# Kernel optimization log

Measured on AMD Instinct MI355X. Metric: run time of the kernel, lower is better.

## Reference

```python
import jax, jax.numpy as jnp
import numpy as np

B, L, DM = 2, 2048, 2048
DI = 2 * DM          # d_inner = expand * d_model
N = 16               # d_state
K = 4                # d_conv
R = DM // 16         # dt_rank = ceil(d_model/16) = 128
FF = 8192            # intermediate_size
EPS = 1e-5


def _silu(x):
    return x * jax.nn.sigmoid(x)


def _ln(x, w, b):
    mu = jnp.mean(x, -1, keepdims=True)
    var = jnp.mean((x - mu) ** 2, -1, keepdims=True)
    return (x - mu) * jax.lax.rsqrt(var + EPS) * w + b


def setup_inputs() -> dict:
    key = jax.random.key(0)
    ks = jax.random.split(key, 8)

    def w(k, shape, fan_in):
        return jax.random.normal(k, shape, jnp.float32) / np.sqrt(fan_in).astype(np.float32)

    return {
        "hidden_states": jax.random.normal(ks[0], (B, L, DM), jnp.float32),
        "ln1_w": jnp.ones((DM,), jnp.float32),
        "ln1_b": jnp.zeros((DM,), jnp.float32),
        "W_in": w(ks[1], (2 * DI, DM), DM),      # in_proj (x and gate merged)
        "conv_w": w(ks[2], (DI, K), K),           # depthwise causal conv weights
        "conv_b": jnp.zeros((DI,), jnp.float32),
        "W_x": w(ks[3], (R + 2 * N, DI), DI),     # x_proj -> [dt_rank | B | C]
        "W_dt": w(ks[4], (DI, R), R),             # dt_proj (bias applied in scan)
        "b_dt": jnp.full((DI,), -2.0, jnp.float32),
        "A": -jnp.tile(jnp.arange(1.0, N + 1.0, dtype=jnp.float32), (DI, 1)),  # (DI, N)
        "Dp": jnp.ones((DI,), jnp.float32),
        "W_out": w(ks[5], (DM, DI), DI),
        "ln2_w": jnp.ones((DM,), jnp.float32),
        "ln2_b": jnp.zeros((DM,), jnp.float32),
        "W_fc1": w(ks[6], (2 * FF, DM), DM),      # GLU: [gate | y]
        "W_fc2": w(ks[7], (DM, FF), FF),
    }


def reference(hidden_states, ln1_w, ln1_b, W_in, conv_w, conv_b, W_x, W_dt, b_dt,
              A, Dp, W_out, ln2_w, ln2_b, W_fc1, W_fc2):
    # --- input layernorm + Phi4Mamba (prefill path: causal_conv1d_fn + selective_scan_fn) ---
    res = hidden_states
    x = _ln(hidden_states, ln1_w, ln1_b)

    xz = jnp.einsum('bld,ed->ble', x, W_in)           # (B, L, 2*DI)
    xs, gate = jnp.split(xz, 2, axis=-1)              # each (B, L, DI)

    # depthwise causal conv1d (width K) fused with silu
    xp = jnp.pad(xs, ((0, 0), (K - 1, 0), (0, 0)))
    conv = conv_b
    for k in range(K):
        conv = conv + xp[:, k:k + L, :] * conv_w[:, k]
    xs = _silu(conv)                                  # (B, L, DI)

    ssm = jnp.einsum('bld,ed->ble', xs, W_x)          # (B, L, R+2N)
    dt, Bm, Cm = ssm[..., :R], ssm[..., R:R + N], ssm[..., R + N:]
    delta = jax.nn.softplus(jnp.einsum('blr,dr->bld', dt, W_dt) + b_dt)  # (B, L, DI)

    def step(h, inp):
        d_t, b_t, c_t, x_t = inp                       # (B,DI),(B,N),(B,N),(B,DI)
        h = jnp.exp(d_t[..., None] * A) * h + (d_t * x_t)[..., None] * b_t[:, None, :]
        return h, jnp.einsum('bdn,bn->bd', h, c_t)

    h0 = jnp.zeros((B, DI, N), xs.dtype)
    _, ys = jax.lax.scan(step, h0, (delta.transpose(1, 0, 2), Bm.transpose(1, 0, 2),
                                    Cm.transpose(1, 0, 2), xs.transpose(1, 0, 2)))
    y = ys.transpose(1, 0, 2) + Dp * xs               # (B, L, DI)
    y = y * _silu(gate)                                # selective_scan z-gating
    attn_out = jnp.einsum('bld,ed->ble', y, W_out)    # (B, L, DM)

    hs = res + attn_out

    # --- post layernorm + GLU MLP ---
    res2 = hs
    x2 = _ln(hs, ln2_w, ln2_b)
    gy = jnp.einsum('bld,ed->ble', x2, W_fc1)         # (B, L, 2*FF)
    g, yy = jnp.split(gy, 2, axis=-1)
    mlp = jnp.einsum('blf,df->bld', yy * _silu(g), W_fc2)
    return res2 + mlp
```

## Files before the change

kernel.cpp:

```cpp
#include <hip/hip_runtime.h>
#include <hip/hip_bf16.h>

typedef unsigned short u16;
typedef unsigned int u32;

#define L_SEQ 2048
#define DMODEL 2048
#define DINNER 4096
#define NSTATE 16
#define MROWS 4096
#define CHUNK 32
#define NCHK  64

typedef __bf16 bf16x8 __attribute__((ext_vector_type(8)));
typedef float f32x4 __attribute__((ext_vector_type(4)));

__device__ __forceinline__ u16 f2bf(float f) {
    union { float f; u32 u; } v; v.f = f;
    u32 u = v.u;
    u32 r = (u + 0x7fffu + ((u >> 16) & 1u)) >> 16;
    return (u16)r;
}
__device__ __forceinline__ float bf2f(u16 h) {
    union { u32 u; float f; } v; v.u = ((u32)h) << 16;
    return v.f;
}

__device__ __forceinline__ void gload16(const void* g, void* l) {
    __builtin_amdgcn_global_load_lds((const __attribute__((address_space(1))) void*)g,
                                     (__attribute__((address_space(3))) void*)l, 16, 0, 0);
}

__global__ __launch_bounds__(256) void cvt_kernel(const float* __restrict__ src,
                                                  u16* __restrict__ dst, long nsrc) {
    long i = ((long)blockIdx.x * 256 + threadIdx.x) * 8;
    union { uint4 v; u16 u[8]; } o;
    if (i < nsrc) {
        f32x4 a = *(const f32x4*)(src + i);
        f32x4 b = *(const f32x4*)(src + i + 4);
#pragma unroll
        for (int j = 0; j < 4; ++j) { o.u[j] = f2bf(a[j]); o.u[4 + j] = f2bf(b[j]); }
    } else {
#pragma unroll
        for (int j = 0; j < 8; ++j) o.u[j] = 0;
    }
    *(uint4*)(dst + i) = o.v;
}

__global__ __launch_bounds__(256) void ln_kernel(const float* __restrict__ in,
                                                 const float* __restrict__ w,
                                                 const float* __restrict__ b,
                                                 u16* __restrict__ out) {
    const long row = blockIdx.x;
    const float* x = in + row * DMODEL;
    const int t = threadIdx.x;
    f32x4 v0 = *(const f32x4*)(x + t * 8);
    f32x4 v1 = *(const f32x4*)(x + t * 8 + 4);
    float s = 0.f, sq = 0.f;
#pragma unroll
    for (int j = 0; j < 4; ++j) {
        s += v0[j] + v1[j];
        sq += v0[j] * v0[j] + v1[j] * v1[j];
    }
#pragma unroll
    for (int off = 32; off > 0; off >>= 1) {
        s += __shfl_down(s, off);
        sq += __shfl_down(sq, off);
    }
    __shared__ float red[8];
    __shared__ float stats[2];
    const int wid = t >> 6, lane = t & 63;
    if (lane == 0) { red[wid] = s; red[4 + wid] = sq; }
    __syncthreads();
    if (t == 0) {
        float S = red[0] + red[1] + red[2] + red[3];
        float Q = red[4] + red[5] + red[6] + red[7];
        float mu = S / (float)DMODEL;
        stats[0] = mu;
        stats[1] = rsqrtf(Q / (float)DMODEL - mu * mu + 1e-5f);
    }
    __syncthreads();
    float mu = stats[0], rstd = stats[1];
    union { uint4 v; u16 u[8]; } o;
#pragma unroll
    for (int j = 0; j < 8; ++j) {
        float xv = (j < 4) ? v0[j] : v1[j - 4];
        o.u[j] = f2bf((xv - mu) * rstd * w[t * 8 + j] + b[t * 8 + j]);
    }
    *(uint4*)(out + row * DMODEL + t * 8) = o.v;
}

template <int MODE>
__global__ __launch_bounds__(256) void gemm_bt(const u16* __restrict__ A,
                                               const u16* __restrict__ W,
                                               float* __restrict__ Cf,
                                               u16* __restrict__ Cb,
                                               const float* __restrict__ addv,
                                               int M, int N, int K, int lda, int ldb) {
    __shared__ u16 As[128 * 64];
    __shared__ u16 Bs[128 * 64];
    const int tid = threadIdx.x;
    const int wid = tid >> 6;
    const int lane = tid & 63;
    const int m0 = blockIdx.y << 7;
    const int n0 = blockIdx.x << 7;
    const long koff = (long)blockIdx.z * K;
    const long zoff = (long)blockIdx.z * M * N;
    const int wr = (wid >> 1) << 6;
    const int wc = (wid & 1) << 6;
    const int l15 = lane & 15;
    const int lhi = lane >> 4;

    f32x4 acc[4][4];
#pragma unroll
    for (int i = 0; i < 4; ++i)
#pragma unroll
        for (int j = 0; j < 4; ++j) acc[i][j] = (f32x4){0.f, 0.f, 0.f, 0.f};

    const int srow = (wid << 3) + (lane >> 3);
    const int scol = (lane & 7) << 3;

    const u16* aBase = A + (long)(m0 + srow) * lda + scol + koff;
    const u16* bBase = W + (long)(n0 + srow) * (long)ldb + scol + koff;

    for (int k0 = 0; k0 < K; k0 += 64) {
#pragma unroll
        for (int i = 0; i < 4; ++i) {
            gload16(aBase + (long)(i * 32) * lda + k0, &As[((i << 5) + (wid << 3)) << 6]);
            gload16(bBase + (long)(i * 32) * ldb + k0, &Bs[((i << 5) + (wid << 3)) << 6]);
        }
        __syncthreads();
#pragma unroll
        for (int kk = 0; kk < 64; kk += 32) {
            bf16x8 af[4], bfr[4];
#pragma unroll
            for (int i = 0; i < 4; ++i)
                af[i] = *(const bf16x8*)&As[((wr + (i << 4) + l15) << 6) + kk + (lhi << 3)];
#pragma unroll
            for (int j = 0; j < 4; ++j)
                bfr[j] = *(const bf16x8*)&Bs[((wc + (j << 4) + l15) << 6) + kk + (lhi << 3)];
#pragma unroll
            for (int i = 0; i < 4; ++i)
#pragma unroll
                for (int j = 0; j < 4; ++j)
                    acc[i][j] = __builtin_amdgcn_mfma_f32_16x16x32_bf16(af[i], bfr[j], acc[i][j], 0, 0, 0);
        }
        __syncthreads();
    }

#pragma unroll
    for (int i = 0; i < 4; ++i) {
#pragma unroll
        for (int j = 0; j < 4; ++j) {
#pragma unroll
            for (int r = 0; r < 4; ++r) {
                int row = m0 + wr + (i << 4) + (lhi << 2) + r;
                int col = n0 + wc + (j << 4) + l15;
                long idx = (long)row * N + col;
                float v = acc[i][j][r];
                if (MODE == 2) v += addv[idx];
                if (MODE == 1) Cb[idx] = f2bf(v);
                else Cf[zoff + idx] = v;
            }
        }
    }
}

template <int MODE>
__global__ __launch_bounds__(512, 2) void gemm8(const u16* __restrict__ A,
                                                const u16* __restrict__ W,
                                                float* __restrict__ Cf,
                                                u16* __restrict__ Cb,
                                                const float* __restrict__ addv,
                                                int M, int N, int K, int lda, int ldb) {
    __shared__ u16 lds[4][2][256 * 32];
    const int tid = threadIdx.x;
    const int wid = tid >> 6;
    const int lane = tid & 63;
    const int wr = wid >> 2;
    const int wc = wid & 3;
    const int l15 = lane & 15;
    const int lhi = lane >> 4;
    const int sw = (l15 >> 1) & 3;
    const long koff = (long)blockIdx.z * K;
    const long zoff = (long)blockIdx.z * M * N;

    const int nwg = gridDim.x * gridDim.y;
    const int flat = blockIdx.y * gridDim.x + blockIdx.x;
    const int q8 = nwg >> 3, r8 = nwg & 7;
    const int xcd = flat & 7, lid = flat >> 3;
    const int swz = (xcd < r8 ? xcd * (q8 + 1) : r8 * (q8 + 1) + (xcd - r8) * q8) + lid;
    const int m0 = (swz / gridDim.x) << 8;
    const int n0 = (swz % gridDim.x) << 8;

    const int srow = lane >> 2;
    const int gc16 = (lane & 3) ^ ((lane >> 3) & 3);

    f32x4 acc[8][4];
#pragma unroll
    for (int i = 0; i < 8; ++i)
#pragma unroll
        for (int j = 0; j < 4; ++j) acc[i][j] = (f32x4){0.f, 0.f, 0.f, 0.f};

#define STAGE_A(t, j)                                                                              \
    gload16(A + (long)(m0 + (j) * 128 + wid * 16 + srow) * lda + koff + (long)(t) * 32 + gc16 * 8, \
            &lds[(t) & 3][0][((j) * 128 + wid * 16) * 32])
#define STAGE_B(t, j)                                                                              \
    gload16(W + (long)(n0 + (j) * 128 + wid * 16 + srow) * (long)ldb + koff + (long)(t) * 32 + gc16 * 8, \
            &lds[(t) & 3][1][((j) * 128 + wid * 16) * 32])

    STAGE_A(0, 0); STAGE_A(0, 1); STAGE_B(0, 0); STAGE_B(0, 1);
    STAGE_A(1, 0); STAGE_A(1, 1); STAGE_B(1, 0); STAGE_B(1, 1);
    STAGE_A(2, 0); STAGE_A(2, 1); STAGE_B(2, 0); STAGE_B(2, 1);
    asm volatile("s_waitcnt vmcnt(8)" ::: "memory");
    __builtin_amdgcn_s_barrier();
    __builtin_amdgcn_sched_barrier(0);

    const int nt = K >> 5;
    for (int t = 0; t < nt; ++t) {
        const u16* Ab = &lds[t & 3][0][0];
        const u16* Bb = &lds[t & 3][1][0];
        bf16x8 afrg[4], bfrg[4];
#pragma unroll
        for (int f = 0; f < 4; ++f)
            afrg[f] = *(const bf16x8*)&Ab[(wr * 128 + f * 16 + l15) * 32 + ((lhi ^ sw) << 3)];
#pragma unroll
        for (int f = 0; f < 4; ++f)
            bfrg[f] = *(const bf16x8*)&Bb[(wc * 64 + f * 16 + l15) * 32 + ((lhi ^ sw) << 3)];
        if (t + 3 < nt) { STAGE_A(t + 3, 0); STAGE_A(t + 3, 1); }
        __builtin_amdgcn_s_barrier();
        __builtin_amdgcn_s_setprio(1);
#pragma unroll
        for (int i = 0; i < 4; ++i)
#pragma unroll
            for (int j = 0; j < 4; ++j)
                acc[i][j] = __builtin_amdgcn_mfma_f32_16x16x32_bf16(afrg[i], bfrg[j], acc[i][j], 0, 0, 0);
        __builtin_amdgcn_s_setprio(0);
#pragma unroll
        for (int f = 0; f < 4; ++f)
            afrg[f] = *(const bf16x8*)&Ab[(wr * 128 + (f + 4) * 16 + l15) * 32 + ((lhi ^ sw) << 3)];
        if (t + 3 < nt) { STAGE_B(t + 3, 0); STAGE_B(t + 3, 1); }
        __builtin_amdgcn_s_barrier();
        __builtin_amdgcn_s_setprio(1);
#pragma unroll
        for (int i = 0; i < 4; ++i)
#pragma unroll
            for (int j = 0; j < 4; ++j)
                acc[i + 4][j] = __builtin_amdgcn_mfma_f32_16x16x32_bf16(afrg[i], bfrg[j], acc[i + 4][j], 0, 0, 0);
        __builtin_amdgcn_s_setprio(0);
        const int rem = nt - 2 - t;
        if (rem >= 2)      { asm volatile("s_waitcnt vmcnt(8)" ::: "memory"); }
        else if (rem == 1) { asm volatile("s_waitcnt vmcnt(4)" ::: "memory"); }
        else if (rem == 0) { asm volatile("s_waitcnt vmcnt(0)" ::: "memory"); }
        __builtin_amdgcn_s_barrier();
        __builtin_amdgcn_sched_barrier(0);
    }
#undef STAGE_A
#undef STAGE_B

#pragma unroll
    for (int i = 0; i < 8; ++i) {
#pragma unroll
        for (int j = 0; j < 4; ++j) {
#pragma unroll
            for (int r = 0; r < 4; ++r) {
                int row = m0 + wr * 128 + i * 16 + lhi * 4 + r;
                int col = n0 + wc * 64 + j * 16 + l15;
                long idx = (long)row * N + col;
                float v = acc[i][j][r];
                if (MODE == 2) v += addv[idx];
                if (MODE == 1) Cb[idx] = f2bf(v);
                else Cf[zoff + idx] = v;
            }
        }
    }
}

__global__ __launch_bounds__(256) void reduce_add_kernel(const float* __restrict__ p0,
                                                         const float* __restrict__ p1,
                                                         const float* __restrict__ add,
                                                         float* __restrict__ out) {
    long i = ((long)blockIdx.x * 256 + threadIdx.x) * 4;
    f32x4 a = *(const f32x4*)(p0 + i);
    f32x4 b = *(const f32x4*)(p1 + i);
    f32x4 c = *(const f32x4*)(add + i);
    f32x4 o;
#pragma unroll
    for (int j = 0; j < 4; ++j) o[j] = a[j] + b[j] + c[j];
    *(f32x4*)(out + i) = o;
}

__global__ __launch_bounds__(256) void reduce4_bf16_kernel(const float* __restrict__ p,
                                                           u16* __restrict__ outb) {
    long i = ((long)blockIdx.x * 256 + threadIdx.x) * 4;
    const long S = 4096L * 256;
    f32x4 a = *(const f32x4*)(p + i);
    f32x4 b = *(const f32x4*)(p + S + i);
    f32x4 c = *(const f32x4*)(p + 2 * S + i);
    f32x4 d = *(const f32x4*)(p + 3 * S + i);
    union { uint2 v; u16 u[4]; } o;
#pragma unroll
    for (int j = 0; j < 4; ++j) o.u[j] = f2bf(a[j] + b[j] + c[j] + d[j]);
    *(uint2*)(outb + i) = o.v;
}

__global__ __launch_bounds__(256) void conv_silu_kernel(const u16* __restrict__ xz,
                                                        const float* __restrict__ cw,
                                                        const float* __restrict__ cb,
                                                        float* __restrict__ xs_out,
                                                        u16* __restrict__ act_out) {
    const int d0 = (blockIdx.x * 256 + threadIdx.x) * 8;
    const int bl = blockIdx.y;
    const int l = bl & (L_SEQ - 1);
    float acc[8];
    float wt[8][4];
#pragma unroll
    for (int j = 0; j < 8; ++j) {
        f32x4 wj = *(const f32x4*)(cw + (d0 + j) * 4);
        wt[j][0] = wj[0]; wt[j][1] = wj[1]; wt[j][2] = wj[2]; wt[j][3] = wj[3];
        acc[j] = cb[d0 + j];
    }
#pragma unroll
    for (int k = 0; k < 4; ++k) {
        int ls = l + k - 3;
        if (ls >= 0) {
            union { uint4 v; u16 u[8]; } xv;
            xv.v = *(const uint4*)(xz + (long)(bl + k - 3) * (2 * DINNER) + d0);
#pragma unroll
            for (int j = 0; j < 8; ++j) acc[j] = fmaf(bf2f(xv.u[j]), wt[j][k], acc[j]);
        }
    }
    union { uint4 v; u16 u[8]; } ob;
    f32x4 o0, o1;
#pragma unroll
    for (int j = 0; j < 8; ++j) {
        float c = acc[j];
        float sv = c / (1.f + __expf(-c));
        if (j < 4) o0[j] = sv; else o1[j - 4] = sv;
        ob.u[j] = f2bf(sv);
    }
    long orow = (long)bl * DINNER + d0;
    *(f32x4*)(xs_out + orow) = o0;
    *(f32x4*)(xs_out + orow + 4) = o1;
    *(uint4*)(act_out + orow) = ob.v;
}

__global__ __launch_bounds__(256) void scan1_kernel(float* __restrict__ dpre,
                                                    const float* __restrict__ xs,
                                                    const u16* __restrict__ ssmb,
                                                    const float* __restrict__ Am,
                                                    const float* __restrict__ bdt,
                                                    float* __restrict__ hend,
                                                    float* __restrict__ sumd) {
    const int d = blockIdx.x * 256 + threadIdx.x;
    const int c = blockIdx.y;
    const int b = blockIdx.z;
    float a2[NSTATE];
#pragma unroll
    for (int n = 0; n < NSTATE; ++n) a2[n] = Am[d * NSTATE + n] * 1.4426950408889634f;
    float h[NSTATE];
#pragma unroll
    for (int n = 0; n < NSTATE; ++n) h[n] = 0.f;
    const float bd = bdt[d];
    float sd = 0.f;
    const long base = (long)b * L_SEQ + (long)c * CHUNK;
    for (int i = 0; i < CHUNK; ++i) {
        const long row = base + i;
        float dpv = dpre[row * DINNER + d] + bd;
        float delta = (dpv > 20.f) ? dpv : log1pf(__expf(dpv));
        dpre[row * DINNER + d] = delta;
        sd += delta;
        float dx = delta * xs[row * DINNER + d];
        const u16* sb = ssmb + row * 256;
#pragma unroll
        for (int n = 0; n < NSTATE; ++n)
            h[n] = __builtin_amdgcn_exp2f(delta * a2[n]) * h[n] + dx * bf2f(sb[128 + n]);
    }
    float* hb = hend + ((long)(b * NCHK + c) * DINNER + d) * NSTATE;
#pragma unroll
    for (int n = 0; n < NSTATE; n += 4)
        *(f32x4*)(hb + n) = (f32x4){h[n], h[n + 1], h[n + 2], h[n + 3]};
    sumd[(long)(b * NCHK + c) * DINNER + d] = sd;
}

__global__ __launch_bounds__(256) void scan2_kernel(float* __restrict__ hend,
                                                    const float* __restrict__ sumd,
                                                    const float* __restrict__ Am) {
    const long idx = (long)blockIdx.x * 256 + threadIdx.x;
    const int n = (int)(idx & 15);
    const int d = (int)((idx >> 4) & (DINNER - 1));
    const int b = (int)(idx >> 16);
    const float a2 = Am[d * NSTATE + n] * 1.4426950408889634f;
    float carry = 0.f;
    for (int c = 0; c < NCHK; ++c) {
        const long soff = (long)(b * NCHK + c) * DINNER + d;
        const long hoff = soff * NSTATE + n;
        float he = hend[hoff];
        float P = __builtin_amdgcn_exp2f(a2 * sumd[soff]);
        hend[hoff] = carry;
        carry = he + P * carry;
    }
}

__global__ __launch_bounds__(256) void scan3_kernel(const float* __restrict__ delta_,
                                                    const float* __restrict__ xs,
                                                    const u16* __restrict__ ssmb,
                                                    const u16* __restrict__ xz,
                                                    const float* __restrict__ Am,
                                                    const float* __restrict__ Dp,
                                                    const float* __restrict__ hinit,
                                                    u16* __restrict__ yb) {
    const int d = blockIdx.x * 256 + threadIdx.x;
    const int c = blockIdx.y;
    const int b = blockIdx.z;
    float a2[NSTATE];
#pragma unroll
    for (int n = 0; n < NSTATE; ++n) a2[n] = Am[d * NSTATE + n] * 1.4426950408889634f;
    float h[NSTATE];
    const float* hb = hinit + ((long)(b * NCHK + c) * DINNER + d) * NSTATE;
#pragma unroll
    for (int n = 0; n < NSTATE; n += 4) {
        f32x4 hv = *(const f32x4*)(hb + n);
        h[n] = hv[0]; h[n + 1] = hv[1]; h[n + 2] = hv[2]; h[n + 3] = hv[3];
    }
    const float dp = Dp[d];
    const long base = (long)b * L_SEQ + (long)c * CHUNK;
    for (int i = 0; i < CHUNK; ++i) {
        const long row = base + i;
        float delta = delta_[row * DINNER + d];
        float xt = xs[row * DINNER + d];
        float dx = delta * xt;
        const u16* sb = ssmb + row * 256;
        float y = 0.f;
#pragma unroll
        for (int n = 0; n < NSTATE; ++n) {
            float Bn = bf2f(sb[128 + n]);
            float Cn = bf2f(sb[144 + n]);
            h[n] = __builtin_amdgcn_exp2f(delta * a2[n]) * h[n] + dx * Bn;
            y = fmaf(h[n], Cn, y);
        }
        float g = bf2f(xz[row * (2 * DINNER) + DINNER + d]);
        float yv = (y + dp * xt) * (g / (1.f + __expf(-g)));
        yb[row * DINNER + d] = f2bf(yv);
    }
}

__global__ __launch_bounds__(256) void gated_act_kernel(const u16* __restrict__ gy,
                                                        u16* __restrict__ actb) {
    long i = ((long)blockIdx.x * 256 + threadIdx.x) * 8;
    long m = i >> 13;
    long f = i & 8191;
    const u16* gp = gy + m * 16384 + f;
    union { uint4 v; u16 u[8]; } gu, yu, ob;
    gu.v = *(const uint4*)gp;
    yu.v = *(const uint4*)(gp + 8192);
#pragma unroll
    for (int j = 0; j < 8; ++j) {
        float g = bf2f(gu.u[j]);
        float yv = bf2f(yu.u[j]);
        ob.u[j] = f2bf(yv * (g / (1.f + __expf(-g))));
    }
    *(uint4*)(actb + i) = ob.v;
}

extern "C" void kernel_launch(void* const* d_in, const int* in_sizes, int n_in,
                              void* d_out, int out_size, void* d_ws, size_t ws_size,
                              hipStream_t stream) {
    const float* hidden = (const float*)d_in[0];
    const float* ln1w   = (const float*)d_in[1];
    const float* ln1b   = (const float*)d_in[2];
    const float* W_in   = (const float*)d_in[3];
    const float* conv_w = (const float*)d_in[4];
    const float* conv_b = (const float*)d_in[5];
    const float* W_x    = (const float*)d_in[6];
    const float* W_dt   = (const float*)d_in[7];
    const float* b_dt   = (const float*)d_in[8];
    const float* Amat   = (const float*)d_in[9];
    const float* Dp     = (const float*)d_in[10];
    const float* W_out  = (const float*)d_in[11];
    const float* ln2w   = (const float*)d_in[12];
    const float* ln2b   = (const float*)d_in[13];
    const float* W_fc1  = (const float*)d_in[14];
    const float* W_fc2  = (const float*)d_in[15];
    float* out = (float*)d_out;

    char* ws = (char*)d_ws;
    const size_t SZ67 = 67108864;
    u16*   ACT   = (u16*)(ws);
    u16*   WB    = (u16*)(ws + SZ67);
    u16*   XZ    = (u16*)(ws + 2 * SZ67);
    float* XS    = (float*)(ws + 3 * SZ67);
    float* DELTA = (float*)(ws + 4 * SZ67);
    u16*   SSMB  = (u16*)(ws + 5 * SZ67);
    float* HS    = (float*)(ws + 5 * SZ67 + 2097152);
    u16*   GY    = XZ;
    float* HEND  = (float*)WB;
    float* SUMD  = (float*)(ws + SZ67 + 33554432);
    float* PART2 = (float*)(ws + SZ67 + 37748736);
    float* PART  = DELTA;

    ln_kernel<<<MROWS, 256, 0, stream>>>(hidden, ln1w, ln1b, ACT);
    cvt_kernel<<<(int)((8192L * 2048) / 2048), 256, 0, stream>>>(W_in, WB, 8192L * 2048);
    gemm8<1><<<dim3(8192 / 256, MROWS / 256), 512, 0, stream>>>(ACT, WB, nullptr, XZ, nullptr,
                                                                MROWS, 8192, 2048, 2048, 2048);
    conv_silu_kernel<<<dim3(2, MROWS), 256, 0, stream>>>(XZ, conv_w, conv_b, XS, ACT);
    cvt_kernel<<<(int)((256L * 4096) / 2048), 256, 0, stream>>>(W_x, WB, 160L * 4096);
    gemm_bt<0><<<dim3(2, 32, 4), 256, 0, stream>>>(ACT, WB, PART2, nullptr, nullptr,
                                                   MROWS, 256, 1024, 4096, 4096);
    reduce4_bf16_kernel<<<1024, 256, 0, stream>>>(PART2, SSMB);
    cvt_kernel<<<(int)((4096L * 128) / 2048), 256, 0, stream>>>(W_dt, WB, 4096L * 128);
    gemm8<0><<<dim3(4096 / 256, MROWS / 256), 512, 0, stream>>>(SSMB, WB, DELTA, nullptr, nullptr,
                                                                MROWS, 4096, 128, 256, 128);
    scan1_kernel<<<dim3(DINNER / 256, NCHK, 2), 256, 0, stream>>>(DELTA, XS, SSMB, Amat, b_dt,
                                                                  HEND, SUMD);
    scan2_kernel<<<(2 * DINNER * NSTATE) / 256, 256, 0, stream>>>(HEND, SUMD, Amat);
    scan3_kernel<<<dim3(DINNER / 256, NCHK, 2), 256, 0, stream>>>(DELTA, XS, SSMB, XZ, Amat, Dp,
                                                                  HEND, ACT);
    cvt_kernel<<<(int)((2048L * 4096) / 2048), 256, 0, stream>>>(W_out, WB, 2048L * 4096);
    gemm8<0><<<dim3(2048 / 256, MROWS / 256, 2), 512, 0, stream>>>(ACT, WB, PART, nullptr, nullptr,
                                                                   MROWS, 2048, 2048, 4096, 4096);
    reduce_add_kernel<<<(int)((4096L * 2048) / 1024), 256, 0, stream>>>(PART, PART + 4096L * 2048,
                                                                        hidden, HS);
    ln_kernel<<<MROWS, 256, 0, stream>>>(HS, ln2w, ln2b, ACT);
    cvt_kernel<<<(int)((16384L * 2048) / 2048), 256, 0, stream>>>(W_fc1, WB, 16384L * 2048);
    gemm8<1><<<dim3(16384 / 256, MROWS / 256), 512, 0, stream>>>(ACT, WB, nullptr, GY, nullptr,
                                                                 MROWS, 16384, 2048, 2048, 2048);
    gated_act_kernel<<<(int)((4096L * 8192) / 2048), 256, 0, stream>>>(GY, ACT);
    cvt_kernel<<<(int)((2048L * 8192) / 2048), 256, 0, stream>>>(W_fc2, WB, 2048L * 8192);
    gemm8<0><<<dim3(2048 / 256, MROWS / 256, 2), 512, 0, stream>>>(ACT, WB, PART, nullptr, nullptr,
                                                                   MROWS, 2048, 4096, 8192, 8192);
    reduce_add_kernel<<<(int)((4096L * 2048) / 1024), 256, 0, stream>>>(PART, PART + 4096L * 2048,
                                                                        HS, out);
}
```

Before: 1.090 ms.

## Fuse split-K reduce with layernorm, drop fp32 conv output, reorder GEMM tile mapping

Merges the split-K reduction plus residual add with the second layernorm into one kernel, so the hidden-state row is not written and re-read. The conv+silu kernel no longer writes a separate fp32 copy of xs, and the scan kernels read the bf16 activation buffer instead, halving that traffic but making the scan input bf16 precision. The gemm8 block swizzle now walks M first within each XCD group instead of N, changing which tiles share L2.

```diff
diff --git a/kernel.cpp b/kernel.cpp
--- a/kernel.cpp
+++ b/kernel.cpp
@@ -88,6 +88,63 @@
         o.u[j] = f2bf((xv - mu) * rstd * w[t * 8 + j] + b[t * 8 + j]);
     }
     *(uint4*)(out + row * DMODEL + t * 8) = o.v;
+}
+
+__global__ __launch_bounds__(256) void reduce_ln_kernel(const float* __restrict__ p0,
+                                                        const float* __restrict__ p1,
+                                                        const float* __restrict__ add,
+                                                        const float* __restrict__ w,
+                                                        const float* __restrict__ b,
+                                                        float* __restrict__ hs_out,
+                                                        u16* __restrict__ ln_out) {
+    const long row = blockIdx.x;
+    const long base = row * DMODEL;
+    const int t = threadIdx.x;
+    f32x4 v0, v1;
+    {
+        f32x4 a0 = *(const f32x4*)(p0 + base + t * 8);
+        f32x4 a1 = *(const f32x4*)(p0 + base + t * 8 + 4);
+        f32x4 b0 = *(const f32x4*)(p1 + base + t * 8);
+        f32x4 b1 = *(const f32x4*)(p1 + base + t * 8 + 4);
+        f32x4 c0 = *(const f32x4*)(add + base + t * 8);
+        f32x4 c1 = *(const f32x4*)(add + base + t * 8 + 4);
+#pragma unroll
+        for (int j = 0; j < 4; ++j) { v0[j] = a0[j] + b0[j] + c0[j]; v1[j] = a1[j] + b1[j] + c1[j]; }
+    }
+    *(f32x4*)(hs_out + base + t * 8) = v0;
+    *(f32x4*)(hs_out + base + t * 8 + 4) = v1;
+    float s = 0.f, sq = 0.f;
+#pragma unroll
+    for (int j = 0; j < 4; ++j) {
+        s += v0[j] + v1[j];
+        sq += v0[j] * v0[j] + v1[j] * v1[j];
+    }
+#pragma unroll
+    for (int off = 32; off > 0; off >>= 1) {
+        s += __shfl_down(s, off);
+        sq += __shfl_down(sq, off);
+    }
+    __shared__ float red[8];
+    __shared__ float stats[2];
+    const int wid = t >> 6, lane = t & 63;
+    if (lane == 0) { red[wid] = s; red[4 + wid] = sq; }
+    __syncthreads();
+    if (t == 0) {
+        float S = red[0] + red[1] + red[2] + red[3];
+        float Q = red[4] + red[5] + red[6] + red[7];
+        float mu = S / (float)DMODEL;
+        stats[0] = mu;
+        stats[1] = rsqrtf(Q / (float)DMODEL - mu * mu + 1e-5f);
+    }
+    __syncthreads();
+    float mu = stats[0], rstd = stats[1];
+    union { uint4 v; u16 u[8]; } o;
+#pragma unroll
+    for (int j = 0; j < 8; ++j) {
+        float xv = (j < 4) ? v0[j] : v1[j - 4];
+        o.u[j] = f2bf((xv - mu) * rstd * w[t * 8 + j] + b[t * 8 + j]);
+    }
+    *(uint4*)(ln_out + base + t * 8) = o.v;
 }
 
 template <int MODE>
@@ -190,8 +247,8 @@
     const int q8 = nwg >> 3, r8 = nwg & 7;
     const int xcd = flat & 7, lid = flat >> 3;
     const int swz = (xcd < r8 ? xcd * (q8 + 1) : r8 * (q8 + 1) + (xcd - r8) * q8) + lid;
-    const int m0 = (swz / gridDim.x) << 8;
-    const int n0 = (swz % gridDim.x) << 8;
+    const int m0 = (swz % gridDim.y) << 8;
+    const int n0 = (swz / gridDim.y) << 8;
 
     const int srow = lane >> 2;
     const int gc16 = (lane & 3) ^ ((lane >> 3) & 3);
@@ -307,7 +364,6 @@
 __global__ __launch_bounds__(256) void conv_silu_kernel(const u16* __restrict__ xz,
                                                         const float* __restrict__ cw,
                                                         const float* __restrict__ cb,
-                                                        float* __restrict__ xs_out,
                                                         u16* __restrict__ act_out) {
     const int d0 = (blockIdx.x * 256 + threadIdx.x) * 8;
     const int bl = blockIdx.y;
@@ -331,22 +387,16 @@
         }
     }
     union { uint4 v; u16 u[8]; } ob;
-    f32x4 o0, o1;
 #pragma unroll
     for (int j = 0; j < 8; ++j) {
         float c = acc[j];
-        float sv = c / (1.f + __expf(-c));
-        if (j < 4) o0[j] = sv; else o1[j - 4] = sv;
-        ob.u[j] = f2bf(sv);
-    }
-    long orow = (long)bl * DINNER + d0;
-    *(f32x4*)(xs_out + orow) = o0;
-    *(f32x4*)(xs_out + orow + 4) = o1;
-    *(uint4*)(act_out + orow) = ob.v;
+        ob.u[j] = f2bf(c / (1.f + __expf(-c)));
+    }
+    *(uint4*)(act_out + (long)bl * DINNER + d0) = ob.v;
 }
 
 __global__ __launch_bounds__(256) void scan1_kernel(float* __restrict__ dpre,
-                                                    const float* __restrict__ xs,
+                                                    const u16* __restrict__ xs,
                                                     const u16* __restrict__ ssmb,
                                                     const float* __restrict__ Am,
                                                     const float* __restrict__ bdt,
@@ -370,7 +420,7 @@
         float delta = (dpv > 20.f) ? dpv : log1pf(__expf(dpv));
         dpre[row * DINNER + d] = delta;
         sd += delta;
-        float dx = delta * xs[row * DINNER + d];
+        float dx = delta * bf2f(xs[row * DINNER + d]);
         const u16* sb = ssmb + row * 256;
 #pragma unroll
         for (int n = 0; n < NSTATE; ++n)
@@ -403,7 +453,7 @@
 }
 
 __global__ __launch_bounds__(256) void scan3_kernel(const float* __restrict__ delta_,
-                                                    const float* __restrict__ xs,
+                                                    const u16* __restrict__ xs,
                                                     const u16* __restrict__ ssmb,
                                                     const u16* __restrict__ xz,
                                                     const float* __restrict__ Am,
@@ -428,7 +478,7 @@
     for (int i = 0; i < CHUNK; ++i) {
         const long row = base + i;
         float delta = delta_[row * DINNER + d];
-        float xt = xs[row * DINNER + d];
+        float xt = bf2f(xs[row * DINNER + d]);
         float dx = delta * xt;
         const u16* sb = ssmb + row * 256;
         float y = 0.f;
@@ -489,7 +539,6 @@
     u16*   ACT   = (u16*)(ws);
     u16*   WB    = (u16*)(ws + SZ67);
     u16*   XZ    = (u16*)(ws + 2 * SZ67);
-    float* XS    = (float*)(ws + 3 * SZ67);
     float* DELTA = (float*)(ws + 4 * SZ67);
     u16*   SSMB  = (u16*)(ws + 5 * SZ67);
     float* HS    = (float*)(ws + 5 * SZ67 + 2097152);
@@ -503,7 +552,7 @@
     cvt_kernel<<<(int)((8192L * 2048) / 2048), 256, 0, stream>>>(W_in, WB, 8192L * 2048);
     gemm8<1><<<dim3(8192 / 256, MROWS / 256), 512, 0, stream>>>(ACT, WB, nullptr, XZ, nullptr,
                                                                 MROWS, 8192, 2048, 2048, 2048);
-    conv_silu_kernel<<<dim3(2, MROWS), 256, 0, stream>>>(XZ, conv_w, conv_b, XS, ACT);
+    conv_silu_kernel<<<dim3(2, MROWS), 256, 0, stream>>>(XZ, conv_w, conv_b, ACT);
     cvt_kernel<<<(int)((256L * 4096) / 2048), 256, 0, stream>>>(W_x, WB, 160L * 4096);
     gemm_bt<0><<<dim3(2, 32, 4), 256, 0, stream>>>(ACT, WB, PART2, nullptr, nullptr,
                                                    MROWS, 256, 1024, 4096, 4096);
@@ -511,17 +560,16 @@
     cvt_kernel<<<(int)((4096L * 128) / 2048), 256, 0, stream>>>(W_dt, WB, 4096L * 128);
     gemm8<0><<<dim3(4096 / 256, MROWS / 256), 512, 0, stream>>>(SSMB, WB, DELTA, nullptr, nullptr,
                                                                 MROWS, 4096, 128, 256, 128);
-    scan1_kernel<<<dim3(DINNER / 256, NCHK, 2), 256, 0, stream>>>(DELTA, XS, SSMB, Amat, b_dt,
+    scan1_kernel<<<dim3(DINNER / 256, NCHK, 2), 256, 0, stream>>>(DELTA, ACT, SSMB, Amat, b_dt,
                                                                   HEND, SUMD);
     scan2_kernel<<<(2 * DINNER * NSTATE) / 256, 256, 0, stream>>>(HEND, SUMD, Amat);
-    scan3_kernel<<<dim3(DINNER / 256, NCHK, 2), 256, 0, stream>>>(DELTA, XS, SSMB, XZ, Amat, Dp,
+    scan3_kernel<<<dim3(DINNER / 256, NCHK, 2), 256, 0, stream>>>(DELTA, ACT, SSMB, XZ, Amat, Dp,
                                                                   HEND, ACT);
     cvt_kernel<<<(int)((2048L * 4096) / 2048), 256, 0, stream>>>(W_out, WB, 2048L * 4096);
     gemm8<0><<<dim3(2048 / 256, MROWS / 256, 2), 512, 0, stream>>>(ACT, WB, PART, nullptr, nullptr,
                                                                    MROWS, 2048, 2048, 4096, 4096);
-    reduce_add_kernel<<<(int)((4096L * 2048) / 1024), 256, 0, stream>>>(PART, PART + 4096L * 2048,
-                                                                        hidden, HS);
-    ln_kernel<<<MROWS, 256, 0, stream>>>(HS, ln2w, ln2b, ACT);
+    reduce_ln_kernel<<<MROWS, 256, 0, stream>>>(PART, PART + 4096L * 2048, hidden,
+                                                ln2w, ln2b, HS, ACT);
     cvt_kernel<<<(int)((16384L * 2048) / 2048), 256, 0, stream>>>(W_fc1, WB, 16384L * 2048);
     gemm8<1><<<dim3(16384 / 256, MROWS / 256), 512, 0, stream>>>(ACT, WB, nullptr, GY, nullptr,
                                                                  MROWS, 16384, 2048, 2048, 2048);
```

After: 1.057 ms. -3.0%, faster.
